# Optimization experiments

Hardware: AMD Instinct MI355X
Metric: run time of the kernel (lower is better)

Reference implementation:

```python
import jax, jax.numpy as jnp
import numpy as np

T, B, V, E = 256, 128, 256, 512
NN = (1024, 1024)  # num_nodes per LSTM layer


def setup_inputs() -> dict:
    key = jax.random.key(0)
    ks = jax.random.split(key, 8)
    inputs = jax.random.normal(ks[0], (T, B, V), jnp.float32)
    emb = jax.random.normal(ks[1], (V, E), jnp.float32) * np.float32(np.sqrt(1.0 / V))
    w0 = jax.random.normal(ks[2], (E + NN[0], 4 * NN[0]), jnp.float32) * np.float32(np.sqrt(1.0 / (E + NN[0])))
    b0 = jnp.zeros((4 * NN[0],), jnp.float32)
    w1 = jax.random.normal(ks[3], (NN[0] + NN[1], 4 * NN[1]), jnp.float32) * np.float32(np.sqrt(1.0 / (NN[0] + NN[1])))
    b1 = jnp.zeros((4 * NN[1],), jnp.float32)
    out_w = jax.random.normal(ks[4], (NN[1], V), jnp.float32) * np.float32(np.sqrt(1.0 / NN[1]))
    out_b = jnp.zeros((V,), jnp.float32)
    return {"inputs": inputs, "embedding_matrix": emb,
            "lstm_w0": w0, "lstm_b0": b0, "lstm_w1": w1, "lstm_b1": b1,
            "out_w": out_w, "out_b": out_b}


def reference(inputs, embedding_matrix, lstm_w0, lstm_b0, lstm_w1, lstm_b1, out_w, out_b):
    Tn, Bn, _ = inputs.shape
    # _embed: (stacked one-hot) @ embedding_matrix -> [T, B, E]
    embs = jnp.einsum('tbv,ve->tbe', inputs, embedding_matrix)
    ws = (lstm_w0, lstm_w1)
    bs = (lstm_b0, lstm_b1)
    init_states = tuple((jnp.zeros((Bn, n), embs.dtype), jnp.zeros((Bn, n), embs.dtype)) for n in NN)

    def step(states, emb):
        out = emb
        new_states = []
        for i in range(len(NN)):
            h, c = states[i]
            n = NN[i]
            # concat([dropout(inp), h]) @ W + b ; dropout_keep_prob = 1.0 -> identity
            lin = jnp.concatenate([out, h], axis=1) @ ws[i] + bs[i]
            f = jax.nn.sigmoid(lin[:, :n])
            ig = jax.nn.sigmoid(lin[:, n:2 * n])
            o = jax.nn.sigmoid(lin[:, 2 * n:3 * n])
            g = jnp.tanh(lin[:, 3 * n:])
            c = f * c + ig * g
            h = o * jnp.tanh(c)
            out = h
            new_states.append((h, c))
        return tuple(new_states), out

    _, rnn_outputs = jax.lax.scan(step, init_states, embs)  # [T, B, NN[-1]]
    # output module: concat over time (axis 0) then single dense layer
    hs = rnn_outputs.reshape(Tn * Bn, NN[-1])
    logits = hs @ out_w + out_b  # [T*B, V]
    return logits
```

## Files before the change

### kernel.cpp

```cpp
#include <hip/hip_runtime.h>
#include <hip/hip_bf16.h>
#include <cstdint>
#include <cstddef>

#define T_STEPS 256
#define BATCH   128
#define VOCAB   256
#define EDIM    512
#define NH      1024
#define GDIM    4096
#define NST0    40
#define NST1    64

typedef __attribute__((ext_vector_type(8))) short short8;
typedef __attribute__((ext_vector_type(4))) float floatx4;

__device__ __forceinline__ float sigmoidf_(float x) { return 1.0f / (1.0f + __expf(-x)); }
__device__ __forceinline__ float tanhf_(float x)    { return 1.0f - 2.0f / (__expf(2.0f * x) + 1.0f); }

typedef __attribute__((address_space(1))) const unsigned int guint;
typedef __attribute__((address_space(3))) unsigned int luint;
__device__ __forceinline__ void load_lds16(const void* g, void* l) {
    __builtin_amdgcn_global_load_lds((guint*)g, (luint*)l, 16, 0, 0);
}

#define BM 128
#define BN 128
#define BK 16
__global__ __launch_bounds__(256) void sgemm_f32(
    const float* __restrict__ A, const float* __restrict__ B,
    float* __restrict__ C, int M, int N, int K)
{
    __shared__ float As[BK][BM + 4];
    __shared__ float Bs[BK][BN + 4];
    const int tid = threadIdx.x;
    const int tr = tid >> 4, tc = tid & 15;
    const int bm = blockIdx.y, bn = blockIdx.x;
    const float* Ab = A + (size_t)bm * BM * K;
    float acc[8][8];
    #pragma unroll
    for (int i = 0; i < 8; ++i)
        #pragma unroll
        for (int j = 0; j < 8; ++j) acc[i][j] = 0.f;
    for (int k0 = 0; k0 < K; k0 += BK) {
        #pragma unroll
        for (int l = 0; l < 2; ++l) {
            int idx = tid + l * 256;
            int row = idx >> 2, c4 = idx & 3;
            float4 v = *(const float4*)(Ab + (size_t)row * K + k0 + c4 * 4);
            As[c4 * 4 + 0][row] = v.x; As[c4 * 4 + 1][row] = v.y;
            As[c4 * 4 + 2][row] = v.z; As[c4 * 4 + 3][row] = v.w;
        }
        #pragma unroll
        for (int l = 0; l < 2; ++l) {
            int idx = tid + l * 256;
            int row = idx >> 5, c4 = idx & 31;
            *(float4*)&Bs[row][c4 * 4] = *(const float4*)(B + (size_t)(k0 + row) * N + bn * BN + c4 * 4);
        }
        __syncthreads();
        #pragma unroll
        for (int kk = 0; kk < BK; ++kk) {
            float4 a0 = *(const float4*)&As[kk][tr * 8];
            float4 a1 = *(const float4*)&As[kk][tr * 8 + 4];
            float4 b0 = *(const float4*)&Bs[kk][tc * 8];
            float4 b1 = *(const float4*)&Bs[kk][tc * 8 + 4];
            float av[8] = {a0.x, a0.y, a0.z, a0.w, a1.x, a1.y, a1.z, a1.w};
            float bv[8] = {b0.x, b0.y, b0.z, b0.w, b1.x, b1.y, b1.z, b1.w};
            #pragma unroll
            for (int i = 0; i < 8; ++i)
                #pragma unroll
                for (int j = 0; j < 8; ++j) acc[i][j] += av[i] * bv[j];
        }
        __syncthreads();
    }
    #pragma unroll
    for (int i = 0; i < 8; ++i) {
        size_t row = (size_t)bm * BM + tr * 8 + i;
        #pragma unroll
        for (int j = 0; j < 8; j += 4) {
            int col = bn * BN + tc * 8 + j;
            *(float4*)(C + row * N + col) =
                make_float4(acc[i][j], acc[i][j+1], acc[i][j+2], acc[i][j+3]);
        }
    }
}

__global__ __launch_bounds__(256) void transpose_to_bf16(
    const float* __restrict__ src, __hip_bfloat16* __restrict__ dst, int R, int C)
{
    __shared__ float t[32][33];
    int x = blockIdx.x * 32 + threadIdx.x;
    #pragma unroll
    for (int i = 0; i < 4; ++i) {
        int y = blockIdx.y * 32 + threadIdx.y + i * 8;
        t[threadIdx.y + i * 8][threadIdx.x] = src[(size_t)y * C + x];
    }
    __syncthreads();
    int x2 = blockIdx.y * 32 + threadIdx.x;
    #pragma unroll
    for (int i = 0; i < 4; ++i) {
        int y2 = blockIdx.x * 32 + threadIdx.y + i * 8;
        dst[(size_t)y2 * R + x2] = __float2bfloat16(t[threadIdx.x][threadIdx.y + i * 8]);
    }
}

__global__ __launch_bounds__(256) void pack_w2(
    const float* __restrict__ src, __hip_bfloat16* __restrict__ dst,
    int koff, int NSTEPS)
{
    __shared__ float t[64][33];
    const int tid = threadIdx.x;
    const int xt = blockIdx.x;
    const int kt = blockIdx.y;
    {
        int yl = tid >> 3;
        int x0 = (tid & 7) * 8;
        const float* p = src + (size_t)(kt * 32 + yl) * GDIM + xt * 64 + x0;
        float4 v0 = *(const float4*)p;
        float4 v1 = *(const float4*)(p + 4);
        t[x0 + 0][yl] = v0.x; t[x0 + 1][yl] = v0.y; t[x0 + 2][yl] = v0.z; t[x0 + 3][yl] = v0.w;
        t[x0 + 4][yl] = v1.x; t[x0 + 5][yl] = v1.y; t[x0 + 6][yl] = v1.z; t[x0 + 7][yl] = v1.w;
    }
    __syncthreads();
    {
        int ll = tid >> 2;
        int quad = tid & 3;
        int lincol = xt * 64 + ll;
        int g = lincol >> 10, n = lincol & 1023;
        int j = n >> 3, c = n & 7;
        int tt = g >> 1;
        int l16 = (g & 1) * 8 + c;
        int s = (koff >> 5) + kt;
        __hip_bfloat16 o[8];
        #pragma unroll
        for (int jj = 0; jj < 8; ++jj)
            o[jj] = __float2bfloat16(t[ll][quad * 8 + jj]);
        size_t off = ((((size_t)j * NSTEPS + s) * 2 + tt) * 64 + (size_t)quad * 16 + l16) * 8;
        *(uint4*)(dst + off) = *(const uint4*)o;
    }
}

__global__ __launch_bounds__(256) void convert_to_bf16(
    const float* __restrict__ src, __hip_bfloat16* __restrict__ dst, size_t n4)
{
    size_t i = (size_t)blockIdx.x * 256 + threadIdx.x;
    if (i < n4) {
        float4 v = *(const float4*)(src + i * 4);
        __hip_bfloat16 o[4] = {__float2bfloat16(v.x), __float2bfloat16(v.y),
                               __float2bfloat16(v.z), __float2bfloat16(v.w)};
        *(uint2*)(dst + i * 4) = *(uint2*)o;
    }
}

#define GKP 40
__global__ __launch_bounds__(256) void gemm_bt(
    const __hip_bfloat16* __restrict__ A, const __hip_bfloat16* __restrict__ Bt,
    const float* __restrict__ bias, float* __restrict__ C, int M, int N, int K)
{
    __shared__ __hip_bfloat16 As[128 * GKP];
    __shared__ __hip_bfloat16 Bs[128 * GKP];
    const int tid = threadIdx.x;
    const int wave = tid >> 6, lane = tid & 63;
    const int quad = lane >> 4, l16 = lane & 15;
    const int wm = (wave >> 1) * 64, wn = (wave & 1) * 64;
    const size_t Arow0 = (size_t)blockIdx.y * 128;
    const size_t Brow0 = (size_t)blockIdx.x * 128;
    floatx4 acc[4][4];
    #pragma unroll
    for (int i = 0; i < 4; ++i)
        #pragma unroll
        for (int j = 0; j < 4; ++j) acc[i][j] = (floatx4)0.f;

    for (int k0 = 0; k0 < K; k0 += 32) {
        #pragma unroll
        for (int l = 0; l < 2; ++l) {
            int idx = tid + l * 256;
            int row = idx >> 2, seg = idx & 3;
            *(uint4*)(As + row * GKP + seg * 8) =
                *(const uint4*)(A + (Arow0 + row) * K + k0 + seg * 8);
            *(uint4*)(Bs + row * GKP + seg * 8) =
                *(const uint4*)(Bt + (Brow0 + row) * K + k0 + seg * 8);
        }
        __syncthreads();
        short8 af[4], bf[4];
        #pragma unroll
        for (int i = 0; i < 4; ++i)
            af[i] = *(const short8*)(As + (wm + i * 16 + l16) * GKP + quad * 8);
        #pragma unroll
        for (int j = 0; j < 4; ++j)
            bf[j] = *(const short8*)(Bs + (wn + j * 16 + l16) * GKP + quad * 8);
        #pragma unroll
        for (int i = 0; i < 4; ++i)
            #pragma unroll
            for (int j = 0; j < 4; ++j)
                acc[i][j] = __builtin_amdgcn_mfma_f32_16x16x32_bf16(af[i], bf[j], acc[i][j], 0, 0, 0);
        __syncthreads();
    }
    #pragma unroll
    for (int i = 0; i < 4; ++i)
        #pragma unroll
        for (int j = 0; j < 4; ++j) {
            int col = (int)Brow0 + wn + j * 16 + l16;
            float bv = bias ? bias[col] : 0.f;
            #pragma unroll
            for (int r = 0; r < 4; ++r) {
                size_t row = Arow0 + wm + i * 16 + quad * 4 + r;
                C[row * N + col] = acc[i][j][r] + bv;
            }
        }
}

template<int NC, int W>
__device__ __forceinline__ void seg_run(
    const __hip_bfloat16* __restrict__ pA,
    const __hip_bfloat16* Wlds, int lane,
    floatx4& acc0, floatx4& acc1)
{
    constexpr int D = (NC < 3) ? NC : 3;
    short8 af[3][8];
    #pragma unroll
    for (int c = 0; c < D; ++c)
        #pragma unroll
        for (int ss = 0; ss < 8; ++ss)
            af[c][ss] = *(const short8*)(pA + (size_t)c * 256 + ss * 32);
    #pragma unroll
    for (int c = 0; c < NC; ++c) {
        #pragma unroll
        for (int ss = 0; ss < 8; ++ss) {
            const int s = (W + c) * 8 + ss;
            short8 bf0 = *(const short8*)&Wlds[s * 1024 + lane * 8];
            short8 bf1 = *(const short8*)&Wlds[s * 1024 + 512 + lane * 8];
            acc0 = __builtin_amdgcn_mfma_f32_16x16x32_bf16(af[c % 3][ss], bf0, acc0, 0, 0, 0);
            acc1 = __builtin_amdgcn_mfma_f32_16x16x32_bf16(af[c % 3][ss], bf1, acc1, 0, 0, 0);
        }
        if (c + 3 < NC) {
            #pragma unroll
            for (int ss = 0; ss < 8; ++ss)
                af[(c + 3) % 3][ss] = *(const short8*)(pA + (size_t)(c + 3) * 256 + ss * 32);
        }
    }
}

__global__ __launch_bounds__(512) void lstm_diag(
    const __hip_bfloat16* __restrict__ inbf,
    const __hip_bfloat16* __restrict__ Wpack0,
    const __hip_bfloat16* __restrict__ Wpack1,
    const float* __restrict__ b0, const float* __restrict__ b1,
    __hip_bfloat16* __restrict__ h0_cur,
    const __hip_bfloat16* __restrict__ h0_prev,
    float* __restrict__ c0, float* __restrict__ c1,
    __hip_bfloat16* __restrict__ H1all,
    int d)
{
    const int bid = blockIdx.x;
    const int layer = (bid >> 3) & 1;
    const int j = ((bid >> 4) << 3) | (bid & 7);
    if (layer == 0 && d >= T_STEPS) return;
    if (layer == 1 && d == 0) return;

    __shared__ __attribute__((aligned(16))) __hip_bfloat16 Wlds[65536];

    const int tid = threadIdx.x;
    const int wave = tid >> 6, lane = tid & 63;
    const int quad = lane >> 4, l16 = lane & 15;

    const __hip_bfloat16 *A0, *A1;
    int A0stride;
    const float* bb; float* cst; __hip_bfloat16* hout;
    bool first;
    if (layer == 0) {
        first = (d == 0);
        bb = b0; cst = c0;
        A0 = inbf + (size_t)d * (BATCH * VOCAB); A0stride = VOCAB;
        A1 = h0_prev;
        hout = h0_cur;
        const __hip_bfloat16* Wp = Wpack0 + (size_t)j * (NST0 * 1024);
        #pragma unroll
        for (int it = 0; it < 10; ++it)
            load_lds16(Wp + it * 4096 + tid * 8, Wlds + it * 4096 + tid * 8);
    } else {
        first = (d == 1);
        bb = b1; cst = c1;
        A0 = h0_prev; A0stride = NH;
        A1 = (d >= 2) ? (H1all + (size_t)(d - 2) * (BATCH * NH)) : h0_prev;
        hout = H1all + (size_t)(d - 1) * (BATCH * NH);
        const __hip_bfloat16* Wp = Wpack1 + (size_t)j * (NST1 * 1024);
        #pragma unroll
        for (int it = 0; it < 16; ++it)
            load_lds16(Wp + it * 4096 + tid * 8, Wlds + it * 4096 + tid * 8);
    }

    const int row = wave * 16 + l16;
    const __hip_bfloat16* pA0 = A0 + (size_t)row * A0stride + quad * 8;
    const __hip_bfloat16* pA1 = A1 + (size_t)row * NH + quad * 8;

    const int cc = j * 8 + (l16 & 7);
    float bv0 = bb[((l16 < 8) ? 0 : 1) * NH + cc];
    float bv1 = bb[((l16 < 8) ? 2 : 3) * NH + cc];
    float cold[4];
    {
        const int bbase = 16 * wave + quad * 4;
        #pragma unroll
        for (int r = 0; r < 4; ++r)
            cold[r] = first ? 0.f : cst[(size_t)(bbase + r) * NH + cc];
    }
    floatx4 acc0 = {bv0, bv0, bv0, bv0};
    floatx4 acc1 = {bv1, bv1, bv1, bv1};

    __syncthreads();
    if (layer == 0) {
        seg_run<1, 0>(pA0, Wlds, lane, acc0, acc1);
        if (!first) seg_run<4, 1>(pA1, Wlds, lane, acc0, acc1);
    } else {
        if (first) {
            seg_run<4, 0>(pA0, Wlds, lane, acc0, acc1);
        } else {
            seg_run<4, 4>(pA1, Wlds, lane, acc0, acc1);
            seg_run<4, 0>(pA0, Wlds, lane, acc0, acc1);
        }
    }

    #pragma unroll
    for (int r = 0; r < 4; ++r) {
        float a0 = acc0[r], a1 = acc1[r];
        float p0 = __shfl_xor(a0, 8, 64);
        float p1 = __shfl_xor(a1, 8, 64);
        if (l16 < 8) {
            int b = 16 * wave + quad * 4 + r;
            float f  = sigmoidf_(a0);
            float ig = sigmoidf_(p0);
            float oo = sigmoidf_(a1);
            float gg = tanhf_(p1);
            size_t idx = (size_t)b * NH + cc;
            float cn = f * cold[r] + ig * gg;
            float hn = oo * tanhf_(cn);
            cst[idx] = cn;
            hout[idx] = __float2bfloat16(hn);
        }
    }
}

__device__ __forceinline__ void spin_wave(const uint32_t* ep, uint32_t target, int lane) {
    asm volatile("" ::: "memory");
    for (;;) {
        uint32_t a = __hip_atomic_load(&ep[lane], __ATOMIC_RELAXED, __HIP_MEMORY_SCOPE_AGENT);
        uint32_t b = __hip_atomic_load(&ep[lane + 64], __ATOMIC_RELAXED, __HIP_MEMORY_SCOPE_AGENT);
        if (__all(a >= target && b >= target)) break;
        __builtin_amdgcn_s_sleep(1);
    }
    asm volatile("" ::: "memory");
}

__device__ __forceinline__ void arrive_ep(uint32_t* slot, uint32_t val) {
    __syncthreads();
    asm volatile("" ::: "memory");
    if (threadIdx.x == 0)
        __hip_atomic_store(slot, val, __ATOMIC_RELAXED, __HIP_MEMORY_SCOPE_AGENT);
}

__global__ void zero_bar(uint32_t* p) { p[threadIdx.x] = 0; }

__device__ __forceinline__ void epilogue_store(
    floatx4 acc0, floatx4 acc1, float* creg, bool first,
    int wave, int quad, int l16, int cc8base,
    __hip_bfloat16* __restrict__ hout)
{
    #pragma unroll
    for (int r = 0; r < 4; ++r) {
        float a0 = acc0[r], a1 = acc1[r];
        float p0 = __shfl_xor(a0, 8, 64);
        float p1 = __shfl_xor(a1, 8, 64);
        float f  = sigmoidf_(a0);
        float ig = sigmoidf_(p0);
        float oo = sigmoidf_(a1);
        float gg = tanhf_(p1);
        float cn = f * (first ? 0.f : creg[r]) + ig * gg;
        if (l16 < 8) creg[r] = cn;
        float hn = oo * tanhf_(cn);
        union { __hip_bfloat16 h; unsigned short u; } cv;
        cv.h = __float2bfloat16(hn);
        unsigned int v1 = (unsigned int)cv.u |
                          (__shfl_xor((unsigned int)cv.u, 1, 64) << 16);
        unsigned int v2 = __shfl_xor(v1, 2, 64);
        unsigned long long p8 = (unsigned long long)v1 |
                                ((unsigned long long)v2 << 32);
        if (l16 == 0 || l16 == 4) {
            int b = 16 * wave + quad * 4 + r;
            __hip_atomic_store((unsigned long long*)&hout[(size_t)b * NH + cc8base + l16],
                               p8, __ATOMIC_RELAXED, __HIP_MEMORY_SCOPE_AGENT);
        }
    }
}

__global__ __launch_bounds__(512, 2) void lstm_persist7(
    const __hip_bfloat16* __restrict__ inbf,
    const __hip_bfloat16* __restrict__ Wpack0,
    const __hip_bfloat16* __restrict__ Wpack1,
    const float* __restrict__ b0, const float* __restrict__ b1,
    __hip_bfloat16* __restrict__ H0all,
    __hip_bfloat16* __restrict__ H1all,
    uint32_t* __restrict__ bar)
{
    __shared__ __attribute__((aligned(16))) float red[32768];

    const int bid = blockIdx.x;
    const int layer = (bid >> 3) & 1;
    const int j = ((bid >> 4) << 3) | (bid & 7);
    const int tid = threadIdx.x;
    const int wv = tid >> 6, lane = tid & 63;
    const int quad = lane >> 4, l16 = lane & 15;

    uint32_t* ep0 = bar;
    uint32_t* ep1 = bar + 128;

    short8 breg[8][2];
    if (layer == 0) {
        const __hip_bfloat16* Wp = Wpack0 + (size_t)j * (NST0 * 1024);
        #pragma unroll
        for (int t = 0; t < 2; ++t)
            breg[0][t] = *(const short8*)(Wp + ((size_t)wv * 2 + t) * 512 + lane * 8);
        #pragma unroll
        for (int i = 0; i < 4; ++i) {
            const int ks = 8 + 4 * wv + i;
            #pragma unroll
            for (int t = 0; t < 2; ++t)
                breg[1 + i][t] = *(const short8*)(Wp + ((size_t)ks * 2 + t) * 512 + lane * 8);
        }
        #pragma unroll
        for (int i = 5; i < 8; ++i) {
            breg[i][0] = breg[0][0];
            breg[i][1] = breg[0][1];
        }
    } else {
        const __hip_bfloat16* Wp = Wpack1 + (size_t)j * (NST1 * 1024);
        #pragma unroll
        for (int i = 0; i < 4; ++i) {
            const int ks1 = 32 + 4 * wv + i;
            const int ks0 = 4 * wv + i;
            #pragma unroll
            for (int t = 0; t < 2; ++t) {
                breg[i][t]     = *(const short8*)(Wp + ((size_t)ks1 * 2 + t) * 512 + lane * 8);
                breg[4 + i][t] = *(const short8*)(Wp + ((size_t)ks0 * 2 + t) * 512 + lane * 8);
            }
        }
    }

    const int cc = j * 8 + (l16 & 7);
    const float* bb = layer ? b1 : b0;
    const float bv0 = bb[((l16 < 8) ? 0 : 1) * NH + cc];
    const float bv1 = bb[((l16 < 8) ? 2 : 3) * NH + cc];
    float creg[4] = {0.f, 0.f, 0.f, 0.f};

    const int hcol = 4 * wv * 32 + quad * 8;
    const int xcol = wv * 32 + quad * 8;

    const int dlo = layer ? 1 : 0;
    const int dhi = layer ? T_STEPS : (T_STEPS - 1);

    for (int d = dlo; d <= dhi; ++d) {
        const bool first = (d == dlo);
        floatx4 acc[8][2];
        #pragma unroll
        for (int m = 0; m < 8; ++m) {
            acc[m][0] = (floatx4)0.f;
            acc[m][1] = (floatx4)0.f;
        }

        __hip_bfloat16* hout;
        if (layer == 0) {
            const __hip_bfloat16* pX = inbf + (size_t)d * (BATCH * VOCAB);
            {
                short8 af[8];
                #pragma unroll
                for (int m = 0; m < 8; ++m)
                    af[m] = *(const short8*)(pX + (size_t)(m * 16 + l16) * VOCAB + xcol);
                #pragma unroll
                for (int m = 0; m < 8; ++m) {
                    acc[m][0] = __builtin_amdgcn_mfma_f32_16x16x32_bf16(af[m], breg[0][0], acc[m][0], 0, 0, 0);
                    acc[m][1] = __builtin_amdgcn_mfma_f32_16x16x32_bf16(af[m], breg[0][1], acc[m][1], 0, 0, 0);
                }
            }
            if (!first) {
                spin_wave(ep0, (uint32_t)d, lane);
                const __hip_bfloat16* pH0 = H0all + (size_t)(d - 1) * (BATCH * NH);
                #pragma unroll
                for (int i = 0; i < 4; ++i) {
                    short8 af[8];
                    #pragma unroll
                    for (int m = 0; m < 8; ++m)
                        af[m] = *(const short8*)(pH0 + (size_t)(m * 16 + l16) * NH + hcol + i * 32);
                    #pragma unroll
                    for (int m = 0; m < 8; ++m) {
                        acc[m][0] = __builtin_amdgcn_mfma_f32_16x16x32_bf16(af[m], breg[1 + i][0], acc[m][0], 0, 0, 0);
                        acc[m][1] = __builtin_amdgcn_mfma_f32_16x16x32_bf16(af[m], breg[1 + i][1], acc[m][1], 0, 0, 0);
                    }
                }
            }
            hout = H0all + (size_t)d * (BATCH * NH);
        } else {
            if (!first) {
                spin_wave(ep1, (uint32_t)(d - 1), lane);
                const __hip_bfloat16* pH1 = H1all + (size_t)(d - 2) * (BATCH * NH);
                #pragma unroll
                for (int i = 0; i < 4; ++i) {
                    short8 af[8];
                    #pragma unroll
                    for (int m = 0; m < 8; ++m)
                        af[m] = *(const short8*)(pH1 + (size_t)(m * 16 + l16) * NH + hcol + i * 32);
                    #pragma unroll
                    for (int m = 0; m < 8; ++m) {
                        acc[m][0] = __builtin_amdgcn_mfma_f32_16x16x32_bf16(af[m], breg[i][0], acc[m][0], 0, 0, 0);
                        acc[m][1] = __builtin_amdgcn_mfma_f32_16x16x32_bf16(af[m], breg[i][1], acc[m][1], 0, 0, 0);
                    }
                }
            }
            spin_wave(ep0, (uint32_t)d, lane);
            const __hip_bfloat16* pH0 = H0all + (size_t)(d - 1) * (BATCH * NH);
            #pragma unroll
            for (int i = 0; i < 4; ++i) {
                short8 af[8];
                #pragma unroll
                for (int m = 0; m < 8; ++m)
                    af[m] = *(const short8*)(pH0 + (size_t)(m * 16 + l16) * NH + hcol + i * 32);
                #pragma unroll
                for (int m = 0; m < 8; ++m) {
                    acc[m][0] = __builtin_amdgcn_mfma_f32_16x16x32_bf16(af[m], breg[4 + i][0], acc[m][0], 0, 0, 0);
                    acc[m][1] = __builtin_amdgcn_mfma_f32_16x16x32_bf16(af[m], breg[4 + i][1], acc[m][1], 0, 0, 0);
                }
            }
            hout = H1all + (size_t)(d - 1) * (BATCH * NH);
        }

        #pragma unroll
        for (int m = 0; m < 8; ++m) {
            *(floatx4*)&red[((((wv * 2 + 0) * 8 + m) * 64) + l16 * 4 + quad) * 4] = acc[m][0];
            *(floatx4*)&red[((((wv * 2 + 1) * 8 + m) * 64) + l16 * 4 + quad) * 4] = acc[m][1];
        }
        __syncthreads();

        floatx4 s0 = (floatx4)0.f, s1 = (floatx4)0.f;
        #pragma unroll
        for (int w = 0; w < 8; ++w) {
            s0 += *(const floatx4*)&red[((((w * 2 + 0) * 8 + wv) * 64) + l16 * 4 + quad) * 4];
            s1 += *(const floatx4*)&red[((((w * 2 + 1) * 8 + wv) * 64) + l16 * 4 + quad) * 4];
        }
        s0 += bv0;
        s1 += bv1;

        epilogue_store(s0, s1, creg, first, wv, quad, l16, j * 8, hout);

        arrive_ep(layer ? &ep1[j] : &ep0[j], (uint32_t)(layer ? d : d + 1));
    }
}

extern "C" void kernel_launch(void* const* d_in, const int* in_sizes, int n_in,
                              void* d_out, int out_size, void* d_ws, size_t ws_size,
                              hipStream_t stream)
{
    const float* inputs = (const float*)d_in[0];
    const float* emb    = (const float*)d_in[1];
    const float* w0     = (const float*)d_in[2];
    const float* b0     = (const float*)d_in[3];
    const float* w1     = (const float*)d_in[4];
    const float* b1     = (const float*)d_in[5];
    const float* outw   = (const float*)d_in[6];
    const float* outb   = (const float*)d_in[7];
    float* out = (float*)d_out;

    char* ws = (char*)d_ws;
    size_t off = 0;
    auto take = [&](size_t bytes) { char* p = ws + off; off += (bytes + 255) & ~(size_t)255; return p; };
    float* Wcomb = (float*)take((size_t)VOCAB * GDIM * 4);
    __hip_bfloat16* Wpack0 = (__hip_bfloat16*)take((size_t)128 * NST0 * 1024 * 2);
    __hip_bfloat16* Wpack1 = (__hip_bfloat16*)take((size_t)128 * NST1 * 1024 * 2);
    __hip_bfloat16* outwt  = (__hip_bfloat16*)take((size_t)NH * VOCAB * 2);
    __hip_bfloat16* inbf   = (__hip_bfloat16*)take((size_t)T_STEPS * BATCH * VOCAB * 2);
    __hip_bfloat16* h0pp0  = (__hip_bfloat16*)take((size_t)BATCH * NH * 2);
    __hip_bfloat16* h0pp1  = (__hip_bfloat16*)take((size_t)BATCH * NH * 2);
    float* c0 = (float*)take((size_t)BATCH * NH * 4);
    float* c1 = (float*)take((size_t)BATCH * NH * 4);
    uint32_t* bar = (uint32_t*)take(1024);
    __hip_bfloat16* H1all  = (__hip_bfloat16*)take((size_t)T_STEPS * BATCH * NH * 2);
    __hip_bfloat16* H0all  = (__hip_bfloat16*)take((size_t)T_STEPS * BATCH * NH * 2);
    const bool ws_ok = (off <= ws_size);

    sgemm_f32<<<dim3(GDIM / BN, VOCAB / BM), 256, 0, stream>>>(
        emb, w0, Wcomb, VOCAB, GDIM, EDIM);
    pack_w2<<<dim3(64, VOCAB / 32), 256, 0, stream>>>(Wcomb, Wpack0, 0, NST0);
    pack_w2<<<dim3(64, NH / 32), 256, 0, stream>>>(w0 + (size_t)EDIM * GDIM, Wpack0, VOCAB, NST0);
    pack_w2<<<dim3(64, NH / 32), 256, 0, stream>>>(w1, Wpack1, 0, NST1);
    pack_w2<<<dim3(64, NH / 32), 256, 0, stream>>>(w1 + (size_t)NH * GDIM, Wpack1, NH, NST1);
    transpose_to_bf16<<<dim3(VOCAB / 32, NH / 32), dim3(32, 8), 0, stream>>>(
        outw, outwt, NH, VOCAB);
    {
        size_t n4 = (size_t)T_STEPS * BATCH * VOCAB / 4;
        convert_to_bf16<<<(int)((n4 + 255) / 256), 256, 0, stream>>>(inputs, inbf, n4);
    }
    zero_bar<<<1, 256, 0, stream>>>(bar);

    bool done = false;
    if (ws_ok) {
        void* args[] = { (void*)&inbf, (void*)&Wpack0, (void*)&Wpack1,
                         (void*)&b0, (void*)&b1,
                         (void*)&H0all, (void*)&H1all, (void*)&bar };
        hipError_t ce = hipLaunchCooperativeKernel(lstm_persist7, dim3(256), dim3(512),
                                                   args, 0u, stream);
        done = (ce == hipSuccess);
    }
    if (!done) {
        for (int d = 0; d <= T_STEPS; ++d) {
            __hip_bfloat16* hcur = (d & 1) ? h0pp1 : h0pp0;
            __hip_bfloat16* hprev = (d & 1) ? h0pp0 : h0pp1;
            lstm_diag<<<256, 512, 0, stream>>>(
                inbf, Wpack0, Wpack1, b0, b1, hcur, hprev, c0, c1, H1all, d);
        }
    }

    gemm_bt<<<dim3(VOCAB / 128, (T_STEPS * BATCH) / 128), 256, 0, stream>>>(
        H1all, outwt, outb, out, T_STEPS * BATCH, VOCAB, NH);
}
```

Before: 5.419 ms.

## Double-buffer h-fragment loads, single-wave spin barrier, contiguous LDS reduction layout

Only wave 0 polls the per-block arrival flags, and the other waves wait at a workgroup barrier, which cuts the atomic polling traffic from every wave. The recurrent h-fragment loads are double-buffered across two register sets so each group's global loads overlap the previous group's MFMAs. The LDS reduction index is also reordered to quad*16+l16 so a wave's stores and loads are contiguous and cause fewer bank conflicts. The extra fragment buffer raises register pressure under launch_bounds(512,2), and the barrier-based spin adds a block-wide sync point.

```diff
diff --git a/kernel.cpp b/kernel.cpp
--- a/kernel.cpp
+++ b/kernel.cpp
@@ -340,14 +340,18 @@
     }
 }
 
-__device__ __forceinline__ void spin_wave(const uint32_t* ep, uint32_t target, int lane) {
+__device__ __forceinline__ void spin_all_ge(const uint32_t* ep, uint32_t target,
+                                            int lane, int wave) {
     asm volatile("" ::: "memory");
-    for (;;) {
-        uint32_t a = __hip_atomic_load(&ep[lane], __ATOMIC_RELAXED, __HIP_MEMORY_SCOPE_AGENT);
-        uint32_t b = __hip_atomic_load(&ep[lane + 64], __ATOMIC_RELAXED, __HIP_MEMORY_SCOPE_AGENT);
-        if (__all(a >= target && b >= target)) break;
-        __builtin_amdgcn_s_sleep(1);
-    }
+    if (wave == 0) {
+        for (;;) {
+            uint32_t a = __hip_atomic_load(&ep[lane], __ATOMIC_RELAXED, __HIP_MEMORY_SCOPE_AGENT);
+            uint32_t b = __hip_atomic_load(&ep[lane + 64], __ATOMIC_RELAXED, __HIP_MEMORY_SCOPE_AGENT);
+            if (__all(a >= target && b >= target)) break;
+            __builtin_amdgcn_s_sleep(1);
+        }
+    }
+    __builtin_amdgcn_s_barrier();
     asm volatile("" ::: "memory");
 }
 
@@ -392,7 +396,7 @@
     }
 }
 
-__global__ __launch_bounds__(512, 2) void lstm_persist7(
+__global__ __launch_bounds__(512, 2) void lstm_persist8(
     const __hip_bfloat16* __restrict__ inbf,
     const __hip_bfloat16* __restrict__ Wpack0,
     const __hip_bfloat16* __restrict__ Wpack1,
@@ -457,6 +461,20 @@
     const int dlo = layer ? 1 : 0;
     const int dhi = layer ? T_STEPS : (T_STEPS - 1);
 
+    #define LOAD_AF(BUF, PBASE, STRIDE, COLBASE, I) do {                         \
+        _Pragma("unroll")                                                        \
+        for (int m_ = 0; m_ < 8; ++m_)                                           \
+            BUF[m_] = *(const short8*)((PBASE) +                                 \
+                (size_t)(m_ * 16 + l16) * (STRIDE) + (COLBASE) + (I) * 32);      \
+    } while (0)
+    #define MFMA_GRP(BUF, WIDX) do {                                             \
+        _Pragma("unroll")                                                        \
+        for (int m_ = 0; m_ < 8; ++m_) {                                         \
+            acc[m_][0] = __builtin_amdgcn_mfma_f32_16x16x32_bf16(BUF[m_], breg[WIDX][0], acc[m_][0], 0, 0, 0); \
+            acc[m_][1] = __builtin_amdgcn_mfma_f32_16x16x32_bf16(BUF[m_], breg[WIDX][1], acc[m_][1], 0, 0, 0); \
+        }                                                                        \
+    } while (0)
+
     for (int d = dlo; d <= dhi; ++d) {
         const bool first = (d == dlo);
         floatx4 acc[8][2];
@@ -466,83 +484,63 @@
             acc[m][1] = (floatx4)0.f;
         }
 
+        short8 afA[8], afB[8];
         __hip_bfloat16* hout;
         if (layer == 0) {
             const __hip_bfloat16* pX = inbf + (size_t)d * (BATCH * VOCAB);
-            {
-                short8 af[8];
-                #pragma unroll
-                for (int m = 0; m < 8; ++m)
-                    af[m] = *(const short8*)(pX + (size_t)(m * 16 + l16) * VOCAB + xcol);
-                #pragma unroll
-                for (int m = 0; m < 8; ++m) {
-                    acc[m][0] = __builtin_amdgcn_mfma_f32_16x16x32_bf16(af[m], breg[0][0], acc[m][0], 0, 0, 0);
-                    acc[m][1] = __builtin_amdgcn_mfma_f32_16x16x32_bf16(af[m], breg[0][1], acc[m][1], 0, 0, 0);
-                }
-            }
+            LOAD_AF(afA, pX, VOCAB, xcol, 0);
+            MFMA_GRP(afA, 0);
             if (!first) {
-                spin_wave(ep0, (uint32_t)d, lane);
+                spin_all_ge(ep0, (uint32_t)d, lane, wv);
                 const __hip_bfloat16* pH0 = H0all + (size_t)(d - 1) * (BATCH * NH);
-                #pragma unroll
-                for (int i = 0; i < 4; ++i) {
-                    short8 af[8];
-                    #pragma unroll
-                    for (int m = 0; m < 8; ++m)
-                        af[m] = *(const short8*)(pH0 + (size_t)(m * 16 + l16) * NH + hcol + i * 32);
-                    #pragma unroll
-                    for (int m = 0; m < 8; ++m) {
-                        acc[m][0] = __builtin_amdgcn_mfma_f32_16x16x32_bf16(af[m], breg[1 + i][0], acc[m][0], 0, 0, 0);
-                        acc[m][1] = __builtin_amdgcn_mfma_f32_16x16x32_bf16(af[m], breg[1 + i][1], acc[m][1], 0, 0, 0);
-                    }
-                }
+                LOAD_AF(afA, pH0, NH, hcol, 0);
+                LOAD_AF(afB, pH0, NH, hcol, 1);
+                MFMA_GRP(afA, 1);
+                LOAD_AF(afA, pH0, NH, hcol, 2);
+                MFMA_GRP(afB, 2);
+                LOAD_AF(afB, pH0, NH, hcol, 3);
+                MFMA_GRP(afA, 3);
+                MFMA_GRP(afB, 4);
             }
             hout = H0all + (size_t)d * (BATCH * NH);
         } else {
             if (!first) {
-                spin_wave(ep1, (uint32_t)(d - 1), lane);
+                spin_all_ge(ep1, (uint32_t)(d - 1), lane, wv);
                 const __hip_bfloat16* pH1 = H1all + (size_t)(d - 2) * (BATCH * NH);
-                #pragma unroll
-                for (int i = 0; i < 4; ++i) {
-                    short8 af[8];
-                    #pragma unroll
-                    for (int m = 0; m < 8; ++m)
-                        af[m] = *(const short8*)(pH1 + (size_t)(m * 16 + l16) * NH + hcol + i * 32);
-                    #pragma unroll
-                    for (int m = 0; m < 8; ++m) {
-                        acc[m][0] = __builtin_amdgcn_mfma_f32_16x16x32_bf16(af[m], breg[i][0], acc[m][0], 0, 0, 0);
-                        acc[m][1] = __builtin_amdgcn_mfma_f32_16x16x32_bf16(af[m], breg[i][1], acc[m][1], 0, 0, 0);
-                    }
-                }
+                LOAD_AF(afA, pH1, NH, hcol, 0);
+                LOAD_AF(afB, pH1, NH, hcol, 1);
+                MFMA_GRP(afA, 0);
+                LOAD_AF(afA, pH1, NH, hcol, 2);
+                MFMA_GRP(afB, 1);
+                LOAD_AF(afB, pH1, NH, hcol, 3);
+                MFMA_GRP(afA, 2);
+                MFMA_GRP(afB, 3);
             }
-            spin_wave(ep0, (uint32_t)d, lane);
+            spin_all_ge(ep0, (uint32_t)d, lane, wv);
             const __hip_bfloat16* pH0 = H0all + (size_t)(d - 1) * (BATCH * NH);
-            #pragma unroll
-            for (int i = 0; i < 4; ++i) {
-                short8 af[8];
-                #pragma unroll
-                for (int m = 0; m < 8; ++m)
-                    af[m] = *(const short8*)(pH0 + (size_t)(m * 16 + l16) * NH + hcol + i * 32);
-                #pragma unroll
-                for (int m = 0; m < 8; ++m) {
-                    acc[m][0] = __builtin_amdgcn_mfma_f32_16x16x32_bf16(af[m], breg[4 + i][0], acc[m][0], 0, 0, 0);
-                    acc[m][1] = __builtin_amdgcn_mfma_f32_16x16x32_bf16(af[m], breg[4 + i][1], acc[m][1], 0, 0, 0);
-                }
-            }
+            LOAD_AF(afA, pH0, NH, hcol, 0);
+            LOAD_AF(afB, pH0, NH, hcol, 1);
+            MFMA_GRP(afA, 4);
+            LOAD_AF(afA, pH0, NH, hcol, 2);
+            MFMA_GRP(afB, 5);
+            LOAD_AF(afB, pH0, NH, hcol, 3);
+            MFMA_GRP(afA, 6);
+            MFMA_GRP(afB, 7);
             hout = H1all + (size_t)(d - 1) * (BATCH * NH);
         }
 
         #pragma unroll
         for (int m = 0; m < 8; ++m) {
-            *(floatx4*)&red[((((wv * 2 + 0) * 8 + m) * 64) + l16 * 4 + quad) * 4] = acc[m][0];
-            *(floatx4*)&red[((((wv * 2 + 1) * 8 + m) * 64) + l16 * 4 + quad) * 4] = acc[m][1];
+            *(floatx4*)&red[((((wv * 2 + 0) * 8 + m) * 64) + quad * 16 + l16) * 4] = acc[m][0];
+            *(floatx4*)&red[((((wv * 2 + 1) * 8 + m) * 64) + quad * 16 + l16) * 4] = acc[m][1];
         }
         __syncthreads();
 
         floatx4 s0 = (floatx4)0.f, s1 = (floatx4)0.f;
         #pragma unroll
         for (int w = 0; w < 8; ++w) {
-            s0 += *(const floatx4*)&red[((((w * 2 + 0) * 8 + wv) * 64) + l16 * 4 + quad) * 4];
-            s1 += *(const floatx4*)&red[((((w * 2 + 1) * 8 + wv) * 64) + l16 * 4 + quad) * 4];
+            s0 += *(const floatx4*)&red[((((w * 2 + 0) * 8 + wv) * 64) + quad * 16 + l16) * 4];
+            s1 += *(const floatx4*)&red[((((w * 2 + 1) * 8 + wv) * 64) + quad * 16 + l16) * 4];
         }
         s0 += bv0;
         s1 += bv1;
@@ -551,6 +549,8 @@
 
         arrive_ep(layer ? &ep1[j] : &ep0[j], (uint32_t)(layer ? d : d + 1));
     }
+    #undef LOAD_AF
+    #undef MFMA_GRP
 }
 
 extern "C" void kernel_launch(void* const* d_in, const int* in_sizes, int n_in,
@@ -603,7 +603,7 @@
         void* args[] = { (void*)&inbf, (void*)&Wpack0, (void*)&Wpack1,
                          (void*)&b0, (void*)&b1,
                          (void*)&H0all, (void*)&H1all, (void*)&bar };
-        hipError_t ce = hipLaunchCooperativeKernel(lstm_persist7, dim3(256), dim3(512),
+        hipError_t ce = hipLaunchCooperativeKernel(lstm_persist8, dim3(256), dim3(512),
                                                    args, 0u, stream);
         done = (ce == hipSuccess);
     }
```

Result: faster. 4.944 ms (-8.8%).
